# Optimization experiments

Hardware: AMD Instinct MI355X
Metric: run time of the kernel (lower is better)

## Reference

```python
import jax, jax.numpy as jnp
import numpy as np

D_MODEL = 2048
NUM_HEADS = 16
KV_HEADS = 4
HEAD_DIM = D_MODEL // NUM_HEADS  # 128
SEQ = 4096
BATCH = 1
ROPE_THETA = 10000.0


def _rope_cache(T, dim, base, dtype):
    inv_freq = 1.0 / (base ** (jnp.arange(0, dim, 2, dtype=jnp.float32) / dim))
    t = jnp.arange(T, dtype=jnp.float32)
    freqs = jnp.outer(t, inv_freq)                      # (T, dim/2)
    emb = jnp.concatenate([freqs, freqs], axis=-1)      # (T, dim)
    return jnp.cos(emb).astype(dtype), jnp.sin(emb).astype(dtype)


def _rotate_half(x):
    d = x.shape[-1] // 2
    return jnp.concatenate([-x[..., d:], x[..., :d]], axis=-1)


def _apply_rope(q, k, cos, sin):
    # q: (B,T,Hq,D), k: (B,T,Hkv,D); cos/sin: (T,D) broadcast over heads
    c = cos[None, :, None, :]
    s = sin[None, :, None, :]
    q = q * c + _rotate_half(q) * s
    k = k * c + _rotate_half(k) * s
    return q, k


def setup_inputs() -> dict:
    key = jax.random.key(0)
    ks = jax.random.split(key, 6)
    sc = 1.0 / np.sqrt(D_MODEL)
    kv_out = KV_HEADS * HEAD_DIM
    return {
        "x": jax.random.normal(ks[0], (BATCH, SEQ, D_MODEL), dtype=jnp.float32),
        "Wq": jax.random.normal(ks[1], (D_MODEL, D_MODEL), dtype=jnp.float32) * sc,
        "Wk": jax.random.normal(ks[2], (D_MODEL, kv_out), dtype=jnp.float32) * sc,
        "Wv": jax.random.normal(ks[3], (D_MODEL, kv_out), dtype=jnp.float32) * sc,
        "Wo": jax.random.normal(ks[4], (D_MODEL, D_MODEL), dtype=jnp.float32) * sc,
        "bo": jax.random.normal(ks[5], (D_MODEL,), dtype=jnp.float32) * 0.01,
    }


def reference(x, Wq, Wk, Wv, Wo, bo):
    B, T, _ = x.shape
    q = (x @ Wq).reshape(B, T, NUM_HEADS, HEAD_DIM)
    k = (x @ Wk).reshape(B, T, KV_HEADS, HEAD_DIM)
    v = (x @ Wv).reshape(B, T, KV_HEADS, HEAD_DIM)

    cos, sin = _rope_cache(T, HEAD_DIM, ROPE_THETA, x.dtype)
    q, k = _apply_rope(q, k, cos, sin)

    reps = NUM_HEADS // KV_HEADS
    k = jnp.repeat(k, reps, axis=2)  # repeat_interleave on head dim
    v = jnp.repeat(v, reps, axis=2)

    # (B,H,T,D)
    q = q.transpose(0, 2, 1, 3)
    k = k.transpose(0, 2, 1, 3)
    v = v.transpose(0, 2, 1, 3)

    scores = jnp.einsum("bhqd,bhkd->bhqk", q, k)
    causal = jnp.triu(jnp.ones((T, T), dtype=bool), k=1)
    scores = jnp.where(causal[None, None], -jnp.inf, scores)
    attn = jax.nn.softmax(scores / jnp.sqrt(jnp.asarray(HEAD_DIM, x.dtype)), axis=-1)

    ctx = jnp.einsum("bhqk,bhkd->bhqd", attn, v)
    ctx = ctx.transpose(0, 2, 1, 3).reshape(B, T, D_MODEL)
    return ctx @ Wo + bo
```

## Files before the change

kernel.cpp:

```cpp
#include <hip/hip_runtime.h>
#include <cstdint>
#include <cstddef>

#define SEQ 4096
#define DM  2048
#define NH  16
#define KVH 4
#define HD  128
#define QSCALE (0.08838834764831845f * 1.4426950408889634f)

typedef short bf16_t;
typedef __attribute__((ext_vector_type(8))) short bf16x8;
typedef __attribute__((ext_vector_type(4))) float f32x4;
typedef __attribute__((ext_vector_type(4))) unsigned uint32x4;

__device__ __forceinline__ bf16_t f2b(float f) {
  unsigned u = __builtin_bit_cast(unsigned, f);
  u += 0x7fffu + ((u >> 16) & 1u);
  return (bf16_t)(u >> 16);
}
__device__ __forceinline__ float b2f(bf16_t s) {
  unsigned u = ((unsigned)(unsigned short)s) << 16;
  return __builtin_bit_cast(float, u);
}
__device__ __forceinline__ unsigned cvtpk(float lo, float hi) {
  unsigned r;
  asm("v_cvt_pk_bf16_f32 %0, %1, %2" : "=v"(r) : "v"(lo), "v"(hi));
  return r;
}

__device__ __forceinline__ void gload_lds16(const void* gsrc, void* ldst) {
  __builtin_amdgcn_global_load_lds(
      (__attribute__((address_space(1))) void*)gsrc,
      (__attribute__((address_space(3))) void*)ldst, 16, 0, 0);
}

__global__ void cast_x_bf16(const float* __restrict__ x, bf16_t* __restrict__ xb, int n4) {
  int i = blockIdx.x * 256 + threadIdx.x;
  if (i >= n4) return;
  float4 v = ((const float4*)x)[i];
  union { bf16_t h[4]; unsigned long long u; } o;
  o.h[0] = f2b(v.x); o.h[1] = f2b(v.y); o.h[2] = f2b(v.z); o.h[3] = f2b(v.w);
  ((unsigned long long*)xb)[i] = o.u;
}

__global__ void transpose_cast_w(const float* __restrict__ W, bf16_t* __restrict__ Wt,
                                 int K, int N) {
  __shared__ float tile[32][33];
  int k0 = blockIdx.y * 32, n0 = blockIdx.x * 32;
  int tx = threadIdx.x, ty = threadIdx.y;
#pragma unroll
  for (int dy = 0; dy < 32; dy += 8)
    tile[ty + dy][tx] = W[(size_t)(k0 + ty + dy) * N + n0 + tx];
  __syncthreads();
#pragma unroll
  for (int dy = 0; dy < 32; dy += 8)
    Wt[(size_t)(n0 + ty + dy) * K + k0 + tx] = f2b(tile[tx][ty + dy]);
}

__global__ void rope_tab(float* __restrict__ ct, float* __restrict__ st) {
  int i = blockIdx.x * 256 + threadIdx.x;
  if (i >= SEQ * 64) return;
  int t = i >> 6, j = i & 63;
  float invf = expf(-(float)j * (9.210340371976184f / 64.0f));
  float ang = (float)t * invf;
  ct[i] = cosf(ang);
  st[i] = sinf(ang);
}

__global__ void rope_apply(bf16_t* __restrict__ Qb, bf16_t* __restrict__ KVb,
                           const float* __restrict__ ct, const float* __restrict__ st) {
  int i = blockIdx.x * 256 + threadIdx.x;
  const int qtot = SEQ * NH * 64;
  const int tot = qtot + SEQ * KVH * 64;
  if (i >= tot) return;
  bf16_t* base; int t, j; float scl;
  if (i < qtot) {
    t = i >> 10; int rem = i & 1023; int hh = rem >> 6; j = rem & 63;
    base = Qb + (size_t)t * DM + hh * HD;
    scl = QSCALE;
  } else {
    int i2 = i - qtot;
    t = i2 >> 8; int rem = i2 & 255; int hh = rem >> 6; j = rem & 63;
    base = KVb + (size_t)t * 1024 + hh * HD;
    scl = 1.0f;
  }
  float c = ct[t * 64 + j], s = st[t * 64 + j];
  float x0 = b2f(base[j]);
  float x1 = b2f(base[j + 64]);
  base[j]      = f2b((x0 * c - x1 * s) * scl);
  base[j + 64] = f2b((x1 * c + x0 * s) * scl);
}

__global__ void transpose_v(const bf16_t* __restrict__ KVb, bf16_t* __restrict__ Vt) {
  __shared__ bf16_t tile[32][33];
  int t0 = blockIdx.y * 32, d0 = blockIdx.x * 32;
  int tx = threadIdx.x, ty = threadIdx.y;
#pragma unroll
  for (int dy = 0; dy < 32; dy += 8)
    tile[ty + dy][tx] = KVb[(size_t)(t0 + ty + dy) * 1024 + 512 + d0 + tx];
  __syncthreads();
  int tt = t0 + tx;
  int j = (tt & ~63) | (tt & 32) | ((tt & 12) << 1) | ((tt & 16) >> 2) | (tt & 3);
#pragma unroll
  for (int dy = 0; dy < 32; dy += 8)
    Vt[(size_t)(d0 + ty + dy) * SEQ + j] = tile[tx][ty + dy];
}

template <int BIAS>
__global__ __launch_bounds__(256, 2)
void gemm_bt(const bf16_t* __restrict__ A, const bf16_t* __restrict__ Bt,
             void* __restrict__ Cout, const float* __restrict__ bias,
             int M, int N, int K) {
  __shared__ __align__(16) bf16_t ldsA[128 * 64];
  __shared__ __align__(16) bf16_t ldsB[128 * 64];
  const int t = threadIdx.x;
  const int w = t >> 6, l = t & 63;
  const int lg = l >> 4, lr = l & 15;
  const int bm = blockIdx.y, bn = blockIdx.x;
  const int wr = (w >> 1) * 64, wc = (w & 1) * 64;

  f32x4 acc[4][4] = {};

  for (int k0 = 0; k0 < K; k0 += 64) {
    __syncthreads();
#pragma unroll
    for (int i = 0; i < 4; ++i) {
      int idx = i * 256 + t;
      int row = idx >> 3;
      int ch  = (idx & 7) ^ (row & 7);
      gload_lds16(A  + (size_t)(bm * 128 + row) * K + k0 + ch * 8, &ldsA[idx * 8]);
      gload_lds16(Bt + (size_t)(bn * 128 + row) * K + k0 + ch * 8, &ldsB[idx * 8]);
    }
    __syncthreads();
#pragma unroll
    for (int kk = 0; kk < 2; ++kk) {
      bf16x8 af[4], bfr[4];
#pragma unroll
      for (int m = 0; m < 4; ++m) {
        int row = wr + m * 16 + lr;
        int ch = (kk * 4 + lg) ^ (row & 7);
        af[m] = *(const bf16x8*)&ldsA[row * 64 + ch * 8];
      }
#pragma unroll
      for (int n = 0; n < 4; ++n) {
        int row = wc + n * 16 + lr;
        int ch = (kk * 4 + lg) ^ (row & 7);
        bfr[n] = *(const bf16x8*)&ldsB[row * 64 + ch * 8];
      }
#pragma unroll
      for (int m = 0; m < 4; ++m)
#pragma unroll
        for (int n = 0; n < 4; ++n)
          acc[m][n] = __builtin_amdgcn_mfma_f32_16x16x32_bf16(af[m], bfr[n], acc[m][n], 0, 0, 0);
    }
  }

  const int row0 = bm * 128 + wr + lg * 4;
  const int col0 = bn * 128 + wc + lr;
  if (BIAS) {
    float* C = (float*)Cout;
#pragma unroll
    for (int n = 0; n < 4; ++n) {
      int col = col0 + n * 16;
      float b = bias[col];
#pragma unroll
      for (int m = 0; m < 4; ++m)
#pragma unroll
        for (int r = 0; r < 4; ++r)
          C[(size_t)(row0 + m * 16 + r) * N + col] = acc[m][n][r] + b;
    }
  } else {
    bf16_t* C = (bf16_t*)Cout;
#pragma unroll
    for (int m = 0; m < 4; ++m)
#pragma unroll
      for (int n = 0; n < 4; ++n) {
        int col = col0 + n * 16;
#pragma unroll
        for (int r = 0; r < 4; ++r)
          C[(size_t)(row0 + m * 16 + r) * N + col] = f2b(acc[m][n][r]);
      }
  }
}

__global__ __launch_bounds__(512, 4)
void attn_fwd(const bf16_t* __restrict__ Qb, const bf16_t* __restrict__ KVb,
              const bf16_t* __restrict__ Vt, bf16_t* __restrict__ ctx) {
  __shared__ __align__(16) bf16_t kt[2][64 * 128];
  __shared__ __align__(16) bf16_t vts[2][128 * 64];

  const int t = threadIdx.x;
  const int w = t >> 6, l = t & 63;
  const int lg = l >> 4, lr = l & 15;
  const int h = blockIdx.y, g = h >> 2;
  const int b = blockIdx.x;
  const int m = w >> 2, wq = w & 3;
  const int qt = m ? 63 - b : b;
  const int qrow0 = qt * 64 + wq * 16;

  bf16x8 qf[4];
#pragma unroll
  for (int kk = 0; kk < 4; ++kk)
    qf[kk] = *(const bf16x8*)&Qb[(size_t)(qrow0 + lr) * DM + h * HD + kk * 32 + lg * 8];

  f32x4 acc[9] = {};
  float m_run = -1e30f;

  bf16x8 ones;
#pragma unroll
  for (int i = 0; i < 8; ++i) ones[i] = (short)0x3F80;

  const bf16_t* ksrc = KVb + g * 128;
  const bf16_t* vsrc = Vt + (size_t)(g * 128) * SEQ;
  auto stage = [&](int buf, int kvt) {
#pragma unroll
    for (int i = 0; i < 2; ++i) {
      int idx = i * 512 + t;
      int row = idx >> 4;
      int ch = (idx & 15) ^ (row & 7);
      gload_lds16(ksrc + (size_t)(kvt * 64 + row) * 1024 + ch * 8, &kt[buf][idx * 8]);
    }
#pragma unroll
    for (int i = 0; i < 2; ++i) {
      int idx = i * 512 + t;
      int row = idx >> 3;
      int ch = (idx & 7) ^ (row & 7);
      gload_lds16(vsrc + (size_t)row * SEQ + kvt * 64 + ch * 8, &vts[buf][idx * 8]);
    }
  };

  const int nkv = 64 - b;
  stage(0, 0);

  for (int kv = 0; kv < nkv; ++kv) {
    const int cur = kv & 1;
    const int kv0 = kv * 64;
    __syncthreads();
    if (kv + 1 < nkv) stage(cur ^ 1, kv + 1);

    if (kv <= qt) {
      f32x4 s[4] = {};
      __builtin_amdgcn_s_setprio(1);
#pragma unroll
      for (int n = 0; n < 4; ++n) {
        int row = n * 16 + lr;
#pragma unroll
        for (int kk = 0; kk < 4; ++kk) {
          int ch = (kk * 4 + lg) ^ (row & 7);
          bf16x8 kf = *(const bf16x8*)&kt[cur][row * 128 + ch * 8];
          s[n] = __builtin_amdgcn_mfma_f32_16x16x32_bf16(kf, qf[kk], s[n], 0, 0, 0);
        }
      }
      __builtin_amdgcn_s_setprio(0);

      const int qrow = qrow0 + lr;
      if (kv == qt) {
#pragma unroll
        for (int n = 0; n < 4; ++n)
#pragma unroll
          for (int r = 0; r < 4; ++r) {
            int key = kv0 + n * 16 + lg * 4 + r;
            if (key > qrow) s[n][r] = -1e30f;
          }
      }

      float pm = s[0][0];
#pragma unroll
      for (int n = 0; n < 4; ++n)
#pragma unroll
        for (int r = 0; r < 4; ++r)
          pm = fmaxf(pm, s[n][r]);
      pm = fmaxf(pm, __shfl_xor(pm, 16, 64));
      pm = fmaxf(pm, __shfl_xor(pm, 32, 64));

      if (__any((int)(pm > m_run + 8.f))) {
        float mn = fmaxf(m_run, pm);
        float a_s = exp2f(m_run - mn);
        m_run = mn;
        float alpha[4];
#pragma unroll
        for (int r = 0; r < 4; ++r)
          alpha[r] = __shfl(a_s, (l & 48) | (lg * 4 + r), 64);
#pragma unroll
        for (int nd = 0; nd < 9; ++nd)
#pragma unroll
          for (int r = 0; r < 4; ++r)
            acc[nd][r] *= alpha[r];
      }

      unsigned u[8];
#pragma unroll
      for (int n = 0; n < 4; ++n) {
        u[2 * n]     = cvtpk(exp2f(s[n][0] - m_run), exp2f(s[n][1] - m_run));
        u[2 * n + 1] = cvtpk(exp2f(s[n][2] - m_run), exp2f(s[n][3] - m_run));
      }
      bf16x8 pf[2];
      pf[0] = __builtin_bit_cast(bf16x8, (uint32x4){u[0], u[1], u[2], u[3]});
      pf[1] = __builtin_bit_cast(bf16x8, (uint32x4){u[4], u[5], u[6], u[7]});

      __builtin_amdgcn_s_setprio(1);
#pragma unroll
      for (int kk2 = 0; kk2 < 2; ++kk2) {
#pragma unroll
        for (int nd = 0; nd < 8; ++nd) {
          int vrow = nd * 16 + lr;
          int vch = (kk2 * 4 + lg) ^ (lr & 7);
          bf16x8 vf = *(const bf16x8*)&vts[cur][vrow * 64 + vch * 8];
          acc[nd] = __builtin_amdgcn_mfma_f32_16x16x32_bf16(pf[kk2], vf, acc[nd], 0, 0, 0);
        }
        acc[8] = __builtin_amdgcn_mfma_f32_16x16x32_bf16(pf[kk2], ones, acc[8], 0, 0, 0);
      }
      __builtin_amdgcn_s_setprio(0);
    }
  }

#pragma unroll
  for (int r = 0; r < 4; ++r) {
    float rl = 1.0f / acc[8][r];
    int qrow = qrow0 + lg * 4 + r;
#pragma unroll
    for (int nd = 0; nd < 8; ++nd) {
      int col = h * HD + nd * 16 + lr;
      ctx[(size_t)qrow * DM + col] = f2b(acc[nd][r] * rl);
    }
  }
}

extern "C" void kernel_launch(void* const* d_in, const int* in_sizes, int n_in,
                              void* d_out, int out_size, void* d_ws, size_t ws_size,
                              hipStream_t stream) {
  const float* x  = (const float*)d_in[0];
  const float* Wq = (const float*)d_in[1];
  const float* Wk = (const float*)d_in[2];
  const float* Wv = (const float*)d_in[3];
  const float* Wo = (const float*)d_in[4];
  const float* bo = (const float*)d_in[5];
  float* out = (float*)d_out;

  char* p = (char*)d_ws;
  bf16_t* xb   = (bf16_t*)p;
  bf16_t* ctx  = xb;
  p += (size_t)SEQ * DM * 2;
  bf16_t* Wqt  = (bf16_t*)p; p += (size_t)DM * DM * 2;
  bf16_t* Wkvt = (bf16_t*)p; p += (size_t)1024 * DM * 2;
  bf16_t* Wot  = (bf16_t*)p; p += (size_t)DM * DM * 2;
  bf16_t* Qb   = (bf16_t*)p; p += (size_t)SEQ * DM * 2;
  bf16_t* KVb  = (bf16_t*)p; p += (size_t)SEQ * 1024 * 2;
  bf16_t* Vt   = (bf16_t*)p; p += (size_t)512 * SEQ * 2;
  float*  ctab = (float*)p;  p += (size_t)SEQ * 64 * 4;
  float*  stab = (float*)p;  p += (size_t)SEQ * 64 * 4;

  cast_x_bf16<<<(SEQ * DM / 4 + 255) / 256, 256, 0, stream>>>(x, xb, SEQ * DM / 4);
  transpose_cast_w<<<dim3(DM / 32, DM / 32), dim3(32, 8), 0, stream>>>(Wq, Wqt, DM, DM);
  transpose_cast_w<<<dim3(512 / 32, DM / 32), dim3(32, 8), 0, stream>>>(Wk, Wkvt, DM, 512);
  transpose_cast_w<<<dim3(512 / 32, DM / 32), dim3(32, 8), 0, stream>>>(Wv, Wkvt + (size_t)512 * DM, DM, 512);
  transpose_cast_w<<<dim3(DM / 32, DM / 32), dim3(32, 8), 0, stream>>>(Wo, Wot, DM, DM);
  rope_tab<<<(SEQ * 64 + 255) / 256, 256, 0, stream>>>(ctab, stab);

  gemm_bt<0><<<dim3(DM / 128, SEQ / 128), 256, 0, stream>>>(xb, Wqt, Qb, nullptr, SEQ, DM, DM);
  gemm_bt<0><<<dim3(1024 / 128, SEQ / 128), 256, 0, stream>>>(xb, Wkvt, KVb, nullptr, SEQ, 1024, DM);

  rope_apply<<<(SEQ * (NH + KVH) * 64 + 255) / 256, 256, 0, stream>>>(Qb, KVb, ctab, stab);
  transpose_v<<<dim3(512 / 32, SEQ / 32), dim3(32, 8), 0, stream>>>(KVb, Vt);

  attn_fwd<<<dim3(32, NH), 512, 0, stream>>>(Qb, KVb, Vt, ctx);

  gemm_bt<1><<<dim3(DM / 128, SEQ / 128), 256, 0, stream>>>(ctx, Wot, out, bo, SEQ, DM, DM);
}
```

Baseline: 275.4 us.

## Switch attention to 32x32x16 MFMA tiles with 4 waves and scalar row-sum

Reworks the attention kernel to use 32x32x16 bf16 MFMAs, with each wave owning 32 query rows and blocks shrunk to 256 threads. The V transpose permutation is changed to match the new P-operand layout. The row sum is now accumulated in registers with a shuffle instead of an extra MFMA against a ones vector. This aims to cut LDS fragment loads per FLOP and drop the redundant ones-MFMA, at the cost of fewer waves per block, larger accumulators and higher register pressure.

After: 309.4 us. 12.4% more time.

```diff
diff --git a/kernel.cpp b/kernel.cpp
--- a/kernel.cpp
+++ b/kernel.cpp
@@ -12,6 +12,7 @@
 typedef short bf16_t;
 typedef __attribute__((ext_vector_type(8))) short bf16x8;
 typedef __attribute__((ext_vector_type(4))) float f32x4;
+typedef __attribute__((ext_vector_type(16))) float f32x16;
 typedef __attribute__((ext_vector_type(4))) unsigned uint32x4;
 
 __device__ __forceinline__ bf16_t f2b(float f) {
@@ -101,7 +102,7 @@
     tile[ty + dy][tx] = KVb[(size_t)(t0 + ty + dy) * 1024 + 512 + d0 + tx];
   __syncthreads();
   int tt = t0 + tx;
-  int j = (tt & ~63) | (tt & 32) | ((tt & 12) << 1) | ((tt & 16) >> 2) | (tt & 3);
+  int j = (tt & ~12) | ((tt & 8) >> 1) | ((tt & 4) << 1);
 #pragma unroll
   for (int dy = 0; dy < 32; dy += 8)
     Vt[(size_t)(d0 + ty + dy) * SEQ + j] = tile[tx][ty + dy];
@@ -184,7 +185,7 @@
   }
 }
 
-__global__ __launch_bounds__(512, 4)
+__global__ __launch_bounds__(256, 2)
 void attn_fwd(const bf16_t* __restrict__ Qb, const bf16_t* __restrict__ KVb,
               const bf16_t* __restrict__ Vt, bf16_t* __restrict__ ctx) {
   __shared__ __align__(16) bf16_t kt[2][64 * 128];
@@ -192,38 +193,34 @@
 
   const int t = threadIdx.x;
   const int w = t >> 6, l = t & 63;
-  const int lg = l >> 4, lr = l & 15;
+  const int lq = l & 31, hi = l >> 5;
   const int h = blockIdx.y, g = h >> 2;
   const int b = blockIdx.x;
-  const int m = w >> 2, wq = w & 3;
-  const int qt = m ? 63 - b : b;
-  const int qrow0 = qt * 64 + wq * 16;
-
-  bf16x8 qf[4];
-#pragma unroll
-  for (int kk = 0; kk < 4; ++kk)
-    qf[kk] = *(const bf16x8*)&Qb[(size_t)(qrow0 + lr) * DM + h * HD + kk * 32 + lg * 8];
-
-  f32x4 acc[9] = {};
-  float m_run = -1e30f;
-
-  bf16x8 ones;
-#pragma unroll
-  for (int i = 0; i < 8; ++i) ones[i] = (short)0x3F80;
+  const int qt = (w >> 1) ? 63 - b : b;
+  const int qrow0 = qt * 64 + (w & 1) * 32;
+  const int q = qrow0 + lq;
+
+  bf16x8 qf[8];
+#pragma unroll
+  for (int ks = 0; ks < 8; ++ks)
+    qf[ks] = *(const bf16x8*)&Qb[(size_t)q * DM + h * HD + ks * 16 + hi * 8];
+
+  f32x16 acc[4] = {};
+  float m_run = -1e30f, l_run = 0.f;
 
   const bf16_t* ksrc = KVb + g * 128;
   const bf16_t* vsrc = Vt + (size_t)(g * 128) * SEQ;
   auto stage = [&](int buf, int kvt) {
 #pragma unroll
-    for (int i = 0; i < 2; ++i) {
-      int idx = i * 512 + t;
+    for (int i = 0; i < 4; ++i) {
+      int idx = i * 256 + t;
       int row = idx >> 4;
       int ch = (idx & 15) ^ (row & 7);
       gload_lds16(ksrc + (size_t)(kvt * 64 + row) * 1024 + ch * 8, &kt[buf][idx * 8]);
     }
 #pragma unroll
-    for (int i = 0; i < 2; ++i) {
-      int idx = i * 512 + t;
+    for (int i = 0; i < 4; ++i) {
+      int idx = i * 256 + t;
       int row = idx >> 3;
       int ch = (idx & 7) ^ (row & 7);
       gload_lds16(vsrc + (size_t)row * SEQ + kvt * 64 + ch * 8, &vts[buf][idx * 8]);
@@ -240,90 +237,97 @@
     if (kv + 1 < nkv) stage(cur ^ 1, kv + 1);
 
     if (kv <= qt) {
-      f32x4 s[4] = {};
+      f32x16 s[2] = {};
       __builtin_amdgcn_s_setprio(1);
 #pragma unroll
-      for (int n = 0; n < 4; ++n) {
-        int row = n * 16 + lr;
-#pragma unroll
-        for (int kk = 0; kk < 4; ++kk) {
-          int ch = (kk * 4 + lg) ^ (row & 7);
+      for (int kti = 0; kti < 2; ++kti) {
+        int row = kti * 32 + lq;
+        int swz = row & 7;
+#pragma unroll
+        for (int ks = 0; ks < 8; ++ks) {
+          int ch = (2 * ks + hi) ^ swz;
           bf16x8 kf = *(const bf16x8*)&kt[cur][row * 128 + ch * 8];
-          s[n] = __builtin_amdgcn_mfma_f32_16x16x32_bf16(kf, qf[kk], s[n], 0, 0, 0);
+          s[kti] = __builtin_amdgcn_mfma_f32_32x32x16_bf16(kf, qf[ks], s[kti], 0, 0, 0);
         }
       }
       __builtin_amdgcn_s_setprio(0);
 
-      const int qrow = qrow0 + lr;
       if (kv == qt) {
 #pragma unroll
-        for (int n = 0; n < 4; ++n)
-#pragma unroll
-          for (int r = 0; r < 4; ++r) {
-            int key = kv0 + n * 16 + lg * 4 + r;
-            if (key > qrow) s[n][r] = -1e30f;
+        for (int kti = 0; kti < 2; ++kti)
+#pragma unroll
+          for (int r = 0; r < 16; ++r) {
+            int key = kv0 + kti * 32 + (r & 3) + 8 * (r >> 2) + 4 * hi;
+            if (key > q) s[kti][r] = -1e30f;
           }
       }
 
       float pm = s[0][0];
 #pragma unroll
-      for (int n = 0; n < 4; ++n)
-#pragma unroll
-        for (int r = 0; r < 4; ++r)
-          pm = fmaxf(pm, s[n][r]);
-      pm = fmaxf(pm, __shfl_xor(pm, 16, 64));
+      for (int kti = 0; kti < 2; ++kti)
+#pragma unroll
+        for (int r = 0; r < 16; ++r)
+          pm = fmaxf(pm, s[kti][r]);
       pm = fmaxf(pm, __shfl_xor(pm, 32, 64));
 
       if (__any((int)(pm > m_run + 8.f))) {
         float mn = fmaxf(m_run, pm);
         float a_s = exp2f(m_run - mn);
         m_run = mn;
-        float alpha[4];
-#pragma unroll
-        for (int r = 0; r < 4; ++r)
-          alpha[r] = __shfl(a_s, (l & 48) | (lg * 4 + r), 64);
-#pragma unroll
-        for (int nd = 0; nd < 9; ++nd)
-#pragma unroll
-          for (int r = 0; r < 4; ++r)
-            acc[nd][r] *= alpha[r];
-      }
-
-      unsigned u[8];
-#pragma unroll
-      for (int n = 0; n < 4; ++n) {
-        u[2 * n]     = cvtpk(exp2f(s[n][0] - m_run), exp2f(s[n][1] - m_run));
-        u[2 * n + 1] = cvtpk(exp2f(s[n][2] - m_run), exp2f(s[n][3] - m_run));
-      }
-      bf16x8 pf[2];
-      pf[0] = __builtin_bit_cast(bf16x8, (uint32x4){u[0], u[1], u[2], u[3]});
-      pf[1] = __builtin_bit_cast(bf16x8, (uint32x4){u[4], u[5], u[6], u[7]});
+        l_run *= a_s;
+        float alpha[16];
+#pragma unroll
+        for (int r = 0; r < 16; ++r)
+          alpha[r] = __shfl(a_s, (r & 3) + 8 * (r >> 2) + 4 * hi, 64);
+#pragma unroll
+        for (int dt = 0; dt < 4; ++dt)
+#pragma unroll
+          for (int r = 0; r < 16; ++r)
+            acc[dt][r] *= alpha[r];
+      }
+
+      float rsum = 0.f;
+      bf16x8 pf[4];
+#pragma unroll
+      for (int kti = 0; kti < 2; ++kti) {
+        float p[16];
+#pragma unroll
+        for (int r = 0; r < 16; ++r) {
+          p[r] = exp2f(s[kti][r] - m_run);
+          rsum += p[r];
+        }
+        pf[2 * kti] = __builtin_bit_cast(bf16x8, (uint32x4){
+            cvtpk(p[0], p[1]), cvtpk(p[2], p[3]), cvtpk(p[4], p[5]), cvtpk(p[6], p[7])});
+        pf[2 * kti + 1] = __builtin_bit_cast(bf16x8, (uint32x4){
+            cvtpk(p[8], p[9]), cvtpk(p[10], p[11]), cvtpk(p[12], p[13]), cvtpk(p[14], p[15])});
+      }
+      rsum += __shfl_xor(rsum, 32, 64);
+      l_run += rsum;
 
       __builtin_amdgcn_s_setprio(1);
 #pragma unroll
-      for (int kk2 = 0; kk2 < 2; ++kk2) {
-#pragma unroll
-        for (int nd = 0; nd < 8; ++nd) {
-          int vrow = nd * 16 + lr;
-          int vch = (kk2 * 4 + lg) ^ (lr & 7);
-          bf16x8 vf = *(const bf16x8*)&vts[cur][vrow * 64 + vch * 8];
-          acc[nd] = __builtin_amdgcn_mfma_f32_16x16x32_bf16(pf[kk2], vf, acc[nd], 0, 0, 0);
+      for (int sstep = 0; sstep < 4; ++sstep) {
+#pragma unroll
+        for (int dt = 0; dt < 4; ++dt) {
+          int row = dt * 32 + lq;
+          int ch = (2 * sstep + hi) ^ (row & 7);
+          bf16x8 vf = *(const bf16x8*)&vts[cur][row * 64 + ch * 8];
+          acc[dt] = __builtin_amdgcn_mfma_f32_32x32x16_bf16(pf[sstep], vf, acc[dt], 0, 0, 0);
         }
-        acc[8] = __builtin_amdgcn_mfma_f32_16x16x32_bf16(pf[kk2], ones, acc[8], 0, 0, 0);
       }
       __builtin_amdgcn_s_setprio(0);
     }
   }
 
 #pragma unroll
-  for (int r = 0; r < 4; ++r) {
-    float rl = 1.0f / acc[8][r];
-    int qrow = qrow0 + lg * 4 + r;
-#pragma unroll
-    for (int nd = 0; nd < 8; ++nd) {
-      int col = h * HD + nd * 16 + lr;
-      ctx[(size_t)qrow * DM + col] = f2b(acc[nd][r] * rl);
-    }
+  for (int r = 0; r < 16; ++r) {
+    int row = (r & 3) + 8 * (r >> 2) + 4 * hi;
+    float ll = __shfl(l_run, row, 64);
+    float rl = 1.0f / ll;
+    int qrow = qrow0 + row;
+#pragma unroll
+    for (int dt = 0; dt < 4; ++dt)
+      ctx[(size_t)qrow * DM + h * HD + dt * 32 + lq] = f2b(acc[dt][r] * rl);
   }
 }
 
@@ -364,7 +368,7 @@
   rope_apply<<<(SEQ * (NH + KVH) * 64 + 255) / 256, 256, 0, stream>>>(Qb, KVb, ctab, stab);
   transpose_v<<<dim3(512 / 32, SEQ / 32), dim3(32, 8), 0, stream>>>(KVb, Vt);
 
-  attn_fwd<<<dim3(32, NH), 512, 0, stream>>>(Qb, KVb, Vt, ctx);
+  attn_fwd<<<dim3(32, NH), 256, 0, stream>>>(Qb, KVb, Vt, ctx);
 
   gemm_bt<1><<<dim3(DM / 128, SEQ / 128), 256, 0, stream>>>(ctx, Wot, out, bo, SEQ, DM, DM);
 }
```
